# Kernel tuning notes

Measured on AMD Instinct MI355X. Metric: run time of the kernel, lower is better.

Reference implementation:

```python
import jax, jax.numpy as jnp
import numpy as np

B, T, K, H = 8, 1024, 512, 8


def setup_inputs() -> dict:
    key = jax.random.key(0)
    kx, kq, kk, kv, ko = jax.random.split(key, 5)
    s = 0.02
    return {
        "x": jax.random.normal(kx, (B, T, K), dtype=jnp.float32),
        "Wq": jax.random.normal(kq, (K * H, K), dtype=jnp.float32) * s,
        "Wk": jax.random.normal(kk, (K * H, K), dtype=jnp.float32) * s,
        "Wv": jax.random.normal(kv, (K * H, K), dtype=jnp.float32) * s,
        "Wo": jax.random.normal(ko, (K, K * H), dtype=jnp.float32) * s,
    }


def reference(x, Wq, Wk, Wv, Wo):
    b, t, k = x.shape
    h = H
    scale = k ** 0.25  # applied to both q and k, total 1/sqrt(k)
    # torch Linear: y = x @ W.T ; view (b,t,h,k) then move heads out: (b,h,t,k)
    def proj(W):
        return (x @ W.T).reshape(b, t, h, k).transpose(0, 2, 1, 3)
    q = proj(Wq) / scale
    kk_ = proj(Wk) / scale
    v = proj(Wv)
    dot = jnp.einsum("bhtd,bhsd->bhts", q, kk_)  # (b,h,t,t)
    # causal mask: strict upper triangle (j > i) -> -inf
    causal = jnp.tril(jnp.ones((t, t), dtype=bool))
    dot = jnp.where(causal[None, None], dot, -jnp.inf)
    attn = jax.nn.softmax(dot, axis=-1)
    out = jnp.einsum("bhts,bhsd->bhtd", attn, v)  # (b,h,t,k)
    out = out.transpose(0, 2, 1, 3).reshape(b, t, h * k)
    return out @ Wo.T
```

## Files before the change

### kernel.cpp

```cpp
#include <hip/hip_runtime.h>
#include <hip/hip_bf16.h>
#include <cstdint>
#include <cmath>


typedef __attribute__((ext_vector_type(8))) short short8;
typedef __attribute__((ext_vector_type(4))) float f32x4;

#define DEVINL __device__ __forceinline__

DEVINL float bf2f(ushort u) { union { uint32_t i; float f; } w; w.i = (uint32_t)u << 16; return w.f; }
DEVINL ushort f2bf(float f) {
  union { float f; uint32_t i; } w; w.f = f;
  uint32_t r = w.i + 0x7FFFu + ((w.i >> 16) & 1u);
  return (ushort)(r >> 16);
}

DEVINL void gl_lds16(const ushort* g, ushort* l) {
  __builtin_amdgcn_global_load_lds(
      (const __attribute__((address_space(1))) uint32_t*)g,
      (__attribute__((address_space(3))) uint32_t*)l, 16, 0, 0);
}

__global__ __launch_bounds__(256) void cvt_f32_bf16(const float* __restrict__ in,
                                                    ushort* __restrict__ out,
                                                    int n8, float scale) {
  int i = blockIdx.x * 256 + threadIdx.x;
  if (i >= n8) return;
  const float4* p = (const float4*)in + (size_t)i * 2;
  float4 a = p[0], b = p[1];
  short8 o;
  o[0] = (short)f2bf(a.x * scale); o[1] = (short)f2bf(a.y * scale);
  o[2] = (short)f2bf(a.z * scale); o[3] = (short)f2bf(a.w * scale);
  o[4] = (short)f2bf(b.x * scale); o[5] = (short)f2bf(b.y * scale);
  o[6] = (short)f2bf(b.z * scale); o[7] = (short)f2bf(b.w * scale);
  ((short8*)out)[i] = o;
}

__global__ __launch_bounds__(256) void zerof4(float4* __restrict__ p, int n4) {
  int i = blockIdx.x * 256 + threadIdx.x;
  if (i < n4) p[i] = float4{0.f, 0.f, 0.f, 0.f};
}

template<bool CSKIP, bool CKB, int EPI, bool ZBH, bool SWZ>
__global__ __launch_bounds__(512, 2) void gemm256(
    const ushort* __restrict__ A0, long long sAb, long long sAh,
    const ushort* __restrict__ B0, long long sBb, long long sBh,
    void* __restrict__ C0, long long sCb, long long sCh,
    int lda, int ldb, int ldc, int K)
{
  int bm, bn;
  if (SWZ) {
    const int X = gridDim.x, nwg = X * gridDim.y;
    const int bid = blockIdx.y * X + blockIdx.x;
    const int cpx = nwg >> 3;
    const int swz = (bid & 7) * cpx + (bid >> 3);
    bm = swz % X; bn = swz / X;
  } else {
    bm = blockIdx.x; bn = blockIdx.y;
  }
  const int bz = blockIdx.z;
  if (CSKIP && bn > bm) return;
  long long za, zb, zc;
  if (ZBH) {
    const long long bi = bz >> 3, hi = bz & 7;
    za = bi * sAb + hi * sAh; zb = bi * sBb + hi * sBh; zc = bi * sCb + hi * sCh;
  } else {
    za = (long long)bz * sAh; zb = (long long)bz * sBh; zc = (long long)bz * sCh;
  }
  const ushort* A = A0 + za;
  const ushort* B = B0 + zb;
  int kend = K;
  if (CKB) { int kb = (bm + 1) * 256; kend = kb < K ? kb : K; }

  __shared__ ushort smem[65536];

  const int tid = threadIdx.x;
  const int wid = tid >> 6, lane = tid & 63;
  const int wr = wid >> 2, wc = wid & 3;
  const int l15 = lane & 15, kq = lane >> 4;

  const int srow8 = lane >> 3;
  const int schunk = ((lane & 7) ^ srow8) * 8;
  const ushort* ag = A + (size_t)(bm * 256 + wid * 8 + srow8) * lda + schunk;
  const ushort* bg = B + (size_t)(bn * 256 + wid * 8 + srow8) * ldb + schunk;

  auto STA = [&](int buf, int band, int kk) {
    gl_lds16(ag + (size_t)band * 64 * lda + kk, &smem[buf * 32768 + band * 4096 + wid * 512]);
  };
  auto STB = [&](int buf, int band, int kk) {
    gl_lds16(bg + (size_t)band * 64 * ldb + kk, &smem[buf * 32768 + 16384 + band * 4096 + wid * 512]);
  };
  auto STAGE8 = [&](int buf, int kk) {
    STB(buf, 0, kk); STB(buf, 1, kk); STB(buf, 2, kk); STB(buf, 3, kk);
    STA(buf, 0, kk); STA(buf, 2, kk); STA(buf, 1, kk); STA(buf, 3, kk);
  };

  f32x4 acc[8][4] = {};
  const int nt = kend >> 6;

  STAGE8(0, 0);

  for (int t = 0; t < nt; ++t) {
    const int cur = t & 1;
    const ushort* As = &smem[cur * 32768];
    const ushort* Bs = As + 16384;
    const bool pre = (t + 1 < nt);

    short8 bq[4], av[4];
    auto LDB = [&](int ks) {
#pragma unroll
      for (int n = 0; n < 4; ++n)
        bq[n] = *(const short8*)
            &Bs[(wc * 64 + n * 16 + l15) * 64 + (((ks * 4 + kq) ^ (l15 & 7)) * 8)];
    };
    auto LDA = [&](int mh, int ks) {
#pragma unroll
      for (int m = 0; m < 4; ++m)
        av[m] = *(const short8*)
            &As[(wr * 128 + mh * 64 + m * 16 + l15) * 64 + (((ks * 4 + kq) ^ (l15 & 7)) * 8)];
    };
    auto MFMAQ = [&](int mh) {
      __builtin_amdgcn_s_setprio(1);
#pragma unroll
      for (int m = 0; m < 4; ++m)
#pragma unroll
        for (int n = 0; n < 4; ++n)
          acc[mh * 4 + m][n] =
              __builtin_amdgcn_mfma_f32_16x16x32_bf16(av[m], bq[n], acc[mh * 4 + m][n], 0, 0, 0);
      __builtin_amdgcn_s_setprio(0);
    };

    if (pre) {
      STAGE8(cur ^ 1, (t + 1) << 6);
      asm volatile("s_waitcnt vmcnt(10)" ::: "memory");
    } else {
      asm volatile("s_waitcnt vmcnt(2)" ::: "memory");
    }
    __builtin_amdgcn_sched_barrier(0);
    __builtin_amdgcn_s_barrier();
    __builtin_amdgcn_sched_barrier(0);
    LDB(0); LDA(0, 0); MFMAQ(0);

    if (pre) asm volatile("s_waitcnt vmcnt(8)" ::: "memory");
    else     asm volatile("s_waitcnt vmcnt(0)" ::: "memory");
    __builtin_amdgcn_sched_barrier(0);
    __builtin_amdgcn_s_barrier();
    __builtin_amdgcn_sched_barrier(0);
    LDA(1, 0); MFMAQ(1);

    LDB(1); LDA(0, 1); MFMAQ(0);

    LDA(1, 1); MFMAQ(1);
    asm volatile("s_waitcnt lgkmcnt(0)" ::: "memory");
    __builtin_amdgcn_sched_barrier(0);
    __builtin_amdgcn_s_barrier();
    __builtin_amdgcn_sched_barrier(0);
  }

  if constexpr (EPI == 0) {
#pragma unroll
    for (int m = 0; m < 8; ++m)
#pragma unroll
      for (int n = 0; n < 4; ++n)
#pragma unroll
        for (int r = 0; r < 4; ++r) {
          const int row = wr * 128 + m * 16 + kq * 4 + r;
          const int col = wc * 64 + n * 16 + l15;
          smem[row * 256 + (((col >> 3) ^ (row & 31)) * 8) + (col & 7)] = f2bf(acc[m][n][r]);
        }
    __syncthreads();
    ushort* C = (ushort*)C0 + zc;
#pragma unroll
    for (int j = 0; j < 16; ++j) {
      const int chi = j * 512 + tid;
      const int row = chi >> 5, cc = chi & 31;
      *(short8*)&C[(size_t)(bm * 256 + row) * ldc + bn * 256 + cc * 8] =
          *(const short8*)&smem[row * 256 + ((cc ^ (row & 31)) * 8)];
    }
  } else {
    float* C = (float*)C0 + zc;
#pragma unroll
    for (int m = 0; m < 8; ++m)
#pragma unroll
      for (int n = 0; n < 4; ++n)
#pragma unroll
        for (int r = 0; r < 4; ++r)
          atomicAdd(&C[(size_t)(bm * 256 + wr * 128 + m * 16 + kq * 4 + r) * ldc
                       + bn * 256 + wc * 64 + n * 16 + l15], acc[m][n][r]);
  }
}

__global__ __launch_bounds__(512, 2) void fused_attn(
    const ushort* __restrict__ QKg, const ushort* __restrict__ Vtg,
    ushort* __restrict__ AOg)
{
  const int nbh = gridDim.y;
  const int lin = blockIdx.y * 8 + blockIdx.x;
  const int bh = lin % nbh;
  const int qb = lin / nbh;
  const int b = bh >> 3, h = bh & 7;

  __shared__ ushort smem[69632];

  const int tid = threadIdx.x;
  const int wid = tid >> 6, lane = tid & 63;
  const int l15 = lane & 15, kq = lane >> 4;

  const ushort* Qb = QKg + (size_t)(b * 1024 + qb * 128 + wid * 16) * 8192 + h * 512;
  const ushort* Kb = QKg + (size_t)b * 1024 * 8192 + 4096 + h * 512;
  const ushort* Vb = Vtg + (size_t)bh * 524288;

  short8 qf[16];
#pragma unroll
  for (int kt = 0; kt < 16; ++kt)
    qf[kt] = *(const short8*)&Qb[(size_t)l15 * 8192 + kt * 32 + kq * 8];

  auto STAGE = [&](int buf, int t) {
    const int s0 = t * 32;
#pragma unroll
    for (int q = 0; q < 4; ++q) {
      const int r = wid * 4 + q;
      const int sc = (lane & 56) | ((lane ^ r) & 7);
      gl_lds16(Kb + (size_t)(s0 + r) * 8192 + sc * 8, &smem[buf * 32768 + r * 512]);
    }
#pragma unroll
    for (int q = 0; q < 4; ++q) {
      const int dbase = wid * 64 + q * 16;
      const int d = dbase + (lane >> 2);
      const int sc = ((lane & 3) ^ ((lane >> 3) & 3)) * 8;
      gl_lds16(Vb + (size_t)d * 1024 + s0 + sc, &smem[buf * 32768 + 16384 + dbase * 32]);
    }
  };

  const int nkv = (qb + 1) * 4;
  const int qrow0 = qb * 128 + wid * 16 + kq * 4;
  float mrow[4] = {-3e38f, -3e38f, -3e38f, -3e38f};
  float lrow[4] = {0.f, 0.f, 0.f, 0.f};
  f32x4 accO[32] = {};
  ushort* PS = &smem[65536 + wid * 512];

  STAGE(0, 0);
  for (int t = 0; t < nkv; ++t) {
    const int cur = t & 1;
    if (t + 1 < nkv) {
      STAGE(cur ^ 1, t + 1);
      asm volatile("s_waitcnt vmcnt(8)" ::: "memory");
    } else {
      asm volatile("s_waitcnt vmcnt(0)" ::: "memory");
    }
    __builtin_amdgcn_sched_barrier(0);
    __builtin_amdgcn_s_barrier();
    __builtin_amdgcn_sched_barrier(0);

    const ushort* KL = &smem[cur * 32768];
    const ushort* VL = KL + 16384;
    const int s0 = t * 32;

    f32x4 sA = {0.f, 0.f, 0.f, 0.f}, sB = {0.f, 0.f, 0.f, 0.f};
    __builtin_amdgcn_s_setprio(1);
#pragma unroll
    for (int kt = 0; kt < 16; ++kt) {
      const int gc = kt * 4 + kq;
      const int pos = ((gc & 56) | ((gc ^ l15) & 7)) * 8;
      short8 k0 = *(const short8*)&KL[l15 * 512 + pos];
      short8 k1 = *(const short8*)&KL[(16 + l15) * 512 + pos];
      sA = __builtin_amdgcn_mfma_f32_16x16x32_bf16(qf[kt], k0, sA, 0, 0, 0);
      sB = __builtin_amdgcn_mfma_f32_16x16x32_bf16(qf[kt], k1, sB, 0, 0, 0);
    }
    __builtin_amdgcn_s_setprio(0);

    float e0v[4], e1v[4], scv[4];
    int grew = 0;
#pragma unroll
    for (int r = 0; r < 4; ++r) {
      float a = sA[r], c = sB[r];
      if (s0 + l15      > qrow0 + r) a = -3e38f;
      if (s0 + 16 + l15 > qrow0 + r) c = -3e38f;
      float mx = fmaxf(a, c);
      mx = fmaxf(mx, __shfl_xor(mx, 1));
      mx = fmaxf(mx, __shfl_xor(mx, 2));
      mx = fmaxf(mx, __shfl_xor(mx, 4));
      mx = fmaxf(mx, __shfl_xor(mx, 8));
      grew |= (mx > mrow[r]);
      const float mn = fmaxf(mrow[r], mx);
      scv[r] = __expf(mrow[r] - mn);
      mrow[r] = mn;
      const float e0 = __expf(a - mn);
      const float e1 = __expf(c - mn);
      float s = e0 + e1;
      s += __shfl_xor(s, 1); s += __shfl_xor(s, 2);
      s += __shfl_xor(s, 4); s += __shfl_xor(s, 8);
      lrow[r] = lrow[r] * scv[r] + s;
      e0v[r] = e0; e1v[r] = e1;
    }
    if (__any(grew)) {
#pragma unroll
      for (int r = 0; r < 4; ++r)
#pragma unroll
        for (int j = 0; j < 32; ++j) accO[j][r] *= scv[r];
    }

#pragma unroll
    for (int r = 0; r < 4; ++r) {
      const int q = kq * 4 + r;
      const int s1 = 16 + l15;
      PS[q * 32 + (((l15 >> 3) ^ (q & 3)) * 8) + (l15 & 7)] = f2bf(e0v[r]);
      PS[q * 32 + (((s1 >> 3) ^ (q & 3)) * 8) + (s1 & 7)]   = f2bf(e1v[r]);
    }
    short8 pa = *(const short8*)&PS[l15 * 32 + ((kq ^ (l15 & 3)) * 8)];

    __builtin_amdgcn_s_setprio(1);
#pragma unroll
    for (int j = 0; j < 32; ++j) {
      short8 bv = *(const short8*)&VL[(j * 16 + l15) * 32 + ((kq ^ ((l15 >> 1) & 3)) * 8)];
      accO[j] = __builtin_amdgcn_mfma_f32_16x16x32_bf16(pa, bv, accO[j], 0, 0, 0);
    }
    __builtin_amdgcn_s_setprio(0);

    asm volatile("s_waitcnt lgkmcnt(0)" ::: "memory");
    __builtin_amdgcn_sched_barrier(0);
    __builtin_amdgcn_s_barrier();
    __builtin_amdgcn_sched_barrier(0);
  }

  ushort* OS = &smem[wid * 8192];
#pragma unroll
  for (int r = 0; r < 4; ++r) {
    const float iv = 1.f / lrow[r];
    const int q = kq * 4 + r;
#pragma unroll
    for (int j = 0; j < 32; ++j) {
      const int col = j * 16 + l15;
      const int ch = col >> 3;
      OS[q * 512 + (((ch & 56) | ((ch ^ q) & 7)) * 8) + (col & 7)] = f2bf(accO[j][r] * iv);
    }
  }
  ushort* AOb = AOg + (size_t)(b * 1024 + qb * 128 + wid * 16) * 4096 + h * 512;
#pragma unroll
  for (int it = 0; it < 16; ++it) {
    const int q = it, c = lane;
    const int pos = (c & 56) | ((c ^ q) & 7);
    *(short8*)&AOb[(size_t)q * 4096 + c * 8] = *(const short8*)&OS[q * 512 + pos * 8];
  }
}

__global__ __launch_bounds__(256) void transposeV(const ushort* __restrict__ Vtmp,
                                                  ushort* __restrict__ Vt) {
  __shared__ ushort tile[64][72];
  const int bx = blockIdx.x;
  const int by = blockIdx.y;
  const int bz = blockIdx.z;
  const int b = bz >> 3, h = bz & 7;
  const int t = threadIdx.x;
  const int r = t >> 2, c = (t & 3) * 16;

  const ushort* src = Vtmp + (size_t)(b * 1024 + bx * 64 + r) * 4096 + h * 512 + by * 64 + c;
  short8 v0 = *(const short8*)src;
  short8 v1 = *(const short8*)(src + 8);
#pragma unroll
  for (int j = 0; j < 8; ++j) { tile[r][c + j] = (ushort)v0[j]; tile[r][c + 8 + j] = (ushort)v1[j]; }
  __syncthreads();

  ushort* dst = Vt + (size_t)(bz * 512 + by * 64 + r) * 1024 + bx * 64 + c;
  short8 o0, o1;
#pragma unroll
  for (int j = 0; j < 8; ++j) { o0[j] = (short)tile[c + j][r]; o1[j] = (short)tile[c + 8 + j][r]; }
  *(short8*)dst = o0;
  *(short8*)(dst + 8) = o1;
}

extern "C" void kernel_launch(void* const* d_in, const int* in_sizes, int n_in,
                              void* d_out, int out_size, void* d_ws, size_t ws_size,
                              hipStream_t stream) {
  const float* x  = (const float*)d_in[0];
  const float* Wq = (const float*)d_in[1];
  const float* Wk = (const float*)d_in[2];
  const float* Wv = (const float*)d_in[3];
  const float* Wo = (const float*)d_in[4];
  float* out = (float*)d_out;

  const int g = (ws_size >= 293601280ull) ? 8 : (ws_size >= 192937984ull) ? 4 : 2;
  const int ng = 8 / g;

  ushort* xb   = (ushort*)d_ws;
  ushort* Wqkv = xb   + (size_t)4194304;
  ushort* Wob  = Wqkv + (size_t)6291456;
  ushort* AO   = Wob  + (size_t)2097152;
  ushort* QKg  = AO   + (size_t)33554432;
  ushort* Vtg  = QKg  + (size_t)g * 8388608;

  const float iscale = (float)(1.0 / pow(512.0, 0.25));

  cvt_f32_bf16<<<2048, 256, 0, stream>>>(x,  xb,             524288, 1.0f);
  cvt_f32_bf16<<<1024, 256, 0, stream>>>(Wq, Wqkv,           262144, iscale);
  cvt_f32_bf16<<<1024, 256, 0, stream>>>(Wk, Wqkv + 2097152, 262144, iscale);
  cvt_f32_bf16<<<1024, 256, 0, stream>>>(Wv, Wqkv + 4194304, 262144, 1.0f);
  cvt_f32_bf16<<<1024, 256, 0, stream>>>(Wo, Wob,            262144, 1.0f);

  for (int grp = 0; grp < ng; ++grp) {
    const ushort* xg = xb + (size_t)grp * g * 524288;
    ushort* AOg = AO + (size_t)grp * g * 4194304;

    gemm256<false, false, 0, false, true><<<dim3(g * 4, 32, 1), 512, 0, stream>>>(
        xg, 0, 0, Wqkv, 0, 0, QKg, 0, 0, 512, 512, 8192, 512);

    gemm256<false, false, 0, false, true><<<dim3(g * 4, 16, 1), 512, 0, stream>>>(
        xg, 0, 0, Wqkv + 4194304, 0, 0, AOg, 0, 0, 512, 512, 4096, 512);

    transposeV<<<dim3(16, 8, 8 * g), 256, 0, stream>>>(AOg, Vtg);

    fused_attn<<<dim3(8, 8 * g), 512, 0, stream>>>(QKg, Vtg, AOg);
  }

  zerof4<<<4096, 256, 0, stream>>>((float4*)out, 1048576);
  gemm256<false, false, 2, false, true><<<dim3(32, 2, 4), 512, 0, stream>>>(
      AO,  0, 1024LL,
      Wob, 0, 1024LL,
      out, 0, 0LL,
      4096, 4096, 512, 1024);
}
```

Before: 590.1 us.

## Give each attention wave two 16-row query tiles, halving block threads

The fused attention kernel drops from 8 to 4 waves per block. Each wave now handles 32 query rows as two 16-row tiles, so every K and V fragment read from LDS feeds two MFMAs, which halves LDS read traffic per FLOP. The cost is roughly double the accumulator registers (two 32-entry f32x4 output sets), which lowers occupancy (launch bounds 256,1) and leaves fewer waves to hide latency. Staging loops and the epilogue are adjusted so each wave covers twice the rows.

```diff
diff --git a/kernel.cpp b/kernel.cpp
--- a/kernel.cpp
+++ b/kernel.cpp
@@ -191,7 +191,7 @@
   }
 }
 
-__global__ __launch_bounds__(512, 2) void fused_attn(
+__global__ __launch_bounds__(256, 1) void fused_attn(
     const ushort* __restrict__ QKg, const ushort* __restrict__ Vtg,
     ushort* __restrict__ AOg)
 {
@@ -207,26 +207,28 @@
   const int wid = tid >> 6, lane = tid & 63;
   const int l15 = lane & 15, kq = lane >> 4;
 
-  const ushort* Qb = QKg + (size_t)(b * 1024 + qb * 128 + wid * 16) * 8192 + h * 512;
+  const ushort* Qb = QKg + (size_t)(b * 1024 + qb * 128 + wid * 32) * 8192 + h * 512;
   const ushort* Kb = QKg + (size_t)b * 1024 * 8192 + 4096 + h * 512;
   const ushort* Vb = Vtg + (size_t)bh * 524288;
 
-  short8 qf[16];
-#pragma unroll
-  for (int kt = 0; kt < 16; ++kt)
-    qf[kt] = *(const short8*)&Qb[(size_t)l15 * 8192 + kt * 32 + kq * 8];
+  short8 qf[2][16];
+#pragma unroll
+  for (int qt = 0; qt < 2; ++qt)
+#pragma unroll
+    for (int kt = 0; kt < 16; ++kt)
+      qf[qt][kt] = *(const short8*)&Qb[(size_t)(qt * 16 + l15) * 8192 + kt * 32 + kq * 8];
 
   auto STAGE = [&](int buf, int t) {
     const int s0 = t * 32;
 #pragma unroll
-    for (int q = 0; q < 4; ++q) {
-      const int r = wid * 4 + q;
+    for (int q = 0; q < 8; ++q) {
+      const int r = wid * 8 + q;
       const int sc = (lane & 56) | ((lane ^ r) & 7);
       gl_lds16(Kb + (size_t)(s0 + r) * 8192 + sc * 8, &smem[buf * 32768 + r * 512]);
     }
 #pragma unroll
-    for (int q = 0; q < 4; ++q) {
-      const int dbase = wid * 64 + q * 16;
+    for (int q = 0; q < 8; ++q) {
+      const int dbase = (wid * 8 + q) * 16;
       const int d = dbase + (lane >> 2);
       const int sc = ((lane & 3) ^ ((lane >> 3) & 3)) * 8;
       gl_lds16(Vb + (size_t)d * 1024 + s0 + sc, &smem[buf * 32768 + 16384 + dbase * 32]);
@@ -234,18 +236,21 @@
   };
 
   const int nkv = (qb + 1) * 4;
-  const int qrow0 = qb * 128 + wid * 16 + kq * 4;
-  float mrow[4] = {-3e38f, -3e38f, -3e38f, -3e38f};
-  float lrow[4] = {0.f, 0.f, 0.f, 0.f};
-  f32x4 accO[32] = {};
-  ushort* PS = &smem[65536 + wid * 512];
+  const int qbase = qb * 128 + wid * 32 + kq * 4;
+  float mrow[2][4], lrow[2][4];
+#pragma unroll
+  for (int qt = 0; qt < 2; ++qt)
+#pragma unroll
+    for (int r = 0; r < 4; ++r) { mrow[qt][r] = -3e38f; lrow[qt][r] = 0.f; }
+  f32x4 accO[2][32] = {};
+  ushort* PS = &smem[65536 + wid * 1024];
 
   STAGE(0, 0);
   for (int t = 0; t < nkv; ++t) {
     const int cur = t & 1;
     if (t + 1 < nkv) {
       STAGE(cur ^ 1, t + 1);
-      asm volatile("s_waitcnt vmcnt(8)" ::: "memory");
+      asm volatile("s_waitcnt vmcnt(16)" ::: "memory");
     } else {
       asm volatile("s_waitcnt vmcnt(0)" ::: "memory");
     }
@@ -257,7 +262,7 @@
     const ushort* VL = KL + 16384;
     const int s0 = t * 32;
 
-    f32x4 sA = {0.f, 0.f, 0.f, 0.f}, sB = {0.f, 0.f, 0.f, 0.f};
+    f32x4 sS[2][2] = {};
     __builtin_amdgcn_s_setprio(1);
 #pragma unroll
     for (int kt = 0; kt < 16; ++kt) {
@@ -265,56 +270,62 @@
       const int pos = ((gc & 56) | ((gc ^ l15) & 7)) * 8;
       short8 k0 = *(const short8*)&KL[l15 * 512 + pos];
       short8 k1 = *(const short8*)&KL[(16 + l15) * 512 + pos];
-      sA = __builtin_amdgcn_mfma_f32_16x16x32_bf16(qf[kt], k0, sA, 0, 0, 0);
-      sB = __builtin_amdgcn_mfma_f32_16x16x32_bf16(qf[kt], k1, sB, 0, 0, 0);
+      sS[0][0] = __builtin_amdgcn_mfma_f32_16x16x32_bf16(qf[0][kt], k0, sS[0][0], 0, 0, 0);
+      sS[0][1] = __builtin_amdgcn_mfma_f32_16x16x32_bf16(qf[0][kt], k1, sS[0][1], 0, 0, 0);
+      sS[1][0] = __builtin_amdgcn_mfma_f32_16x16x32_bf16(qf[1][kt], k0, sS[1][0], 0, 0, 0);
+      sS[1][1] = __builtin_amdgcn_mfma_f32_16x16x32_bf16(qf[1][kt], k1, sS[1][1], 0, 0, 0);
     }
     __builtin_amdgcn_s_setprio(0);
 
-    float e0v[4], e1v[4], scv[4];
+    float scv[2][4];
     int grew = 0;
 #pragma unroll
-    for (int r = 0; r < 4; ++r) {
-      float a = sA[r], c = sB[r];
-      if (s0 + l15      > qrow0 + r) a = -3e38f;
-      if (s0 + 16 + l15 > qrow0 + r) c = -3e38f;
-      float mx = fmaxf(a, c);
-      mx = fmaxf(mx, __shfl_xor(mx, 1));
-      mx = fmaxf(mx, __shfl_xor(mx, 2));
-      mx = fmaxf(mx, __shfl_xor(mx, 4));
-      mx = fmaxf(mx, __shfl_xor(mx, 8));
-      grew |= (mx > mrow[r]);
-      const float mn = fmaxf(mrow[r], mx);
-      scv[r] = __expf(mrow[r] - mn);
-      mrow[r] = mn;
-      const float e0 = __expf(a - mn);
-      const float e1 = __expf(c - mn);
-      float s = e0 + e1;
-      s += __shfl_xor(s, 1); s += __shfl_xor(s, 2);
-      s += __shfl_xor(s, 4); s += __shfl_xor(s, 8);
-      lrow[r] = lrow[r] * scv[r] + s;
-      e0v[r] = e0; e1v[r] = e1;
+    for (int qt = 0; qt < 2; ++qt) {
+#pragma unroll
+      for (int r = 0; r < 4; ++r) {
+        float a = sS[qt][0][r], c = sS[qt][1][r];
+        const int qrow = qbase + qt * 16 + r;
+        if (s0 + l15      > qrow) a = -3e38f;
+        if (s0 + 16 + l15 > qrow) c = -3e38f;
+        float mx = fmaxf(a, c);
+        mx = fmaxf(mx, __shfl_xor(mx, 1));
+        mx = fmaxf(mx, __shfl_xor(mx, 2));
+        mx = fmaxf(mx, __shfl_xor(mx, 4));
+        mx = fmaxf(mx, __shfl_xor(mx, 8));
+        grew |= (mx > mrow[qt][r]);
+        const float mn = fmaxf(mrow[qt][r], mx);
+        scv[qt][r] = __expf(mrow[qt][r] - mn);
+        mrow[qt][r] = mn;
+        const float e0 = __expf(a - mn);
+        const float e1 = __expf(c - mn);
+        float s = e0 + e1;
+        s += __shfl_xor(s, 1); s += __shfl_xor(s, 2);
+        s += __shfl_xor(s, 4); s += __shfl_xor(s, 8);
+        lrow[qt][r] = lrow[qt][r] * scv[qt][r] + s;
+        const int q = qt * 16 + kq * 4 + r;
+        const int s1 = 16 + l15;
+        PS[q * 32 + (((l15 >> 3) ^ (q & 3)) * 8) + (l15 & 7)] = f2bf(e0);
+        PS[q * 32 + (((s1 >> 3) ^ (q & 3)) * 8) + (s1 & 7)]   = f2bf(e1);
+      }
     }
     if (__any(grew)) {
 #pragma unroll
-      for (int r = 0; r < 4; ++r)
-#pragma unroll
-        for (int j = 0; j < 32; ++j) accO[j][r] *= scv[r];
-    }
-
-#pragma unroll
-    for (int r = 0; r < 4; ++r) {
-      const int q = kq * 4 + r;
-      const int s1 = 16 + l15;
-      PS[q * 32 + (((l15 >> 3) ^ (q & 3)) * 8) + (l15 & 7)] = f2bf(e0v[r]);
-      PS[q * 32 + (((s1 >> 3) ^ (q & 3)) * 8) + (s1 & 7)]   = f2bf(e1v[r]);
-    }
-    short8 pa = *(const short8*)&PS[l15 * 32 + ((kq ^ (l15 & 3)) * 8)];
+      for (int qt = 0; qt < 2; ++qt)
+#pragma unroll
+        for (int r = 0; r < 4; ++r)
+#pragma unroll
+          for (int j = 0; j < 32; ++j) accO[qt][j][r] *= scv[qt][r];
+    }
+
+    short8 pa0 = *(const short8*)&PS[l15 * 32 + ((kq ^ (l15 & 3)) * 8)];
+    short8 pa1 = *(const short8*)&PS[(16 + l15) * 32 + ((kq ^ (l15 & 3)) * 8)];
 
     __builtin_amdgcn_s_setprio(1);
 #pragma unroll
     for (int j = 0; j < 32; ++j) {
       short8 bv = *(const short8*)&VL[(j * 16 + l15) * 32 + ((kq ^ ((l15 >> 1) & 3)) * 8)];
-      accO[j] = __builtin_amdgcn_mfma_f32_16x16x32_bf16(pa, bv, accO[j], 0, 0, 0);
+      accO[0][j] = __builtin_amdgcn_mfma_f32_16x16x32_bf16(pa0, bv, accO[0][j], 0, 0, 0);
+      accO[1][j] = __builtin_amdgcn_mfma_f32_16x16x32_bf16(pa1, bv, accO[1][j], 0, 0, 0);
     }
     __builtin_amdgcn_s_setprio(0);
 
@@ -324,24 +335,26 @@
     __builtin_amdgcn_sched_barrier(0);
   }
 
-  ushort* OS = &smem[wid * 8192];
-#pragma unroll
-  for (int r = 0; r < 4; ++r) {
-    const float iv = 1.f / lrow[r];
-    const int q = kq * 4 + r;
-#pragma unroll
-    for (int j = 0; j < 32; ++j) {
-      const int col = j * 16 + l15;
-      const int ch = col >> 3;
-      OS[q * 512 + (((ch & 56) | ((ch ^ q) & 7)) * 8) + (col & 7)] = f2bf(accO[j][r] * iv);
-    }
-  }
-  ushort* AOb = AOg + (size_t)(b * 1024 + qb * 128 + wid * 16) * 4096 + h * 512;
-#pragma unroll
-  for (int it = 0; it < 16; ++it) {
-    const int q = it, c = lane;
-    const int pos = (c & 56) | ((c ^ q) & 7);
-    *(short8*)&AOb[(size_t)q * 4096 + c * 8] = *(const short8*)&OS[q * 512 + pos * 8];
+  ushort* OS = &smem[wid * 16384];
+#pragma unroll
+  for (int qt = 0; qt < 2; ++qt)
+#pragma unroll
+    for (int r = 0; r < 4; ++r) {
+      const float iv = 1.f / lrow[qt][r];
+      const int q = qt * 16 + kq * 4 + r;
+#pragma unroll
+      for (int j = 0; j < 32; ++j) {
+        const int col = j * 16 + l15;
+        const int ch = col >> 3;
+        OS[q * 512 + (((ch & 56) | ((ch ^ q) & 7)) * 8) + (col & 7)] = f2bf(accO[qt][j][r] * iv);
+      }
+    }
+  ushort* AOb = AOg + (size_t)(b * 1024 + qb * 128 + wid * 32) * 4096 + h * 512;
+#pragma unroll
+  for (int it = 0; it < 32; ++it) {
+    const int c = lane;
+    const int pos = (c & 56) | ((c ^ it) & 7);
+    *(short8*)&AOb[(size_t)it * 4096 + c * 8] = *(const short8*)&OS[it * 512 + pos * 8];
   }
 }
 
@@ -410,7 +423,7 @@
 
     transposeV<<<dim3(16, 8, 8 * g), 256, 0, stream>>>(AOg, Vtg);
 
-    fused_attn<<<dim3(8, 8 * g), 512, 0, stream>>>(QKg, Vtg, AOg);
+    fused_attn<<<dim3(8, 8 * g), 256, 0, stream>>>(QKg, Vtg, AOg);
   }
 
   zerof4<<<4096, 256, 0, stream>>>((float4*)out, 1048576);
```

Result: slower. 1.891 ms (+220.5%).
